# Kernel tuning notes

Hardware: AMD Instinct MI355X
Metric: run time of the kernel (lower is better)

Reference implementation:

```python
import jax, jax.numpy as jnp
import numpy as np
from jax import lax

D, H, DH, F, K, L, N = 512, 8, 64, 2048, 31, 512, 16
EPS = 1e-5

def layer_norm(x, g, b):
    m = x.mean(-1, keepdims=True)
    v = ((x - m) ** 2).mean(-1, keepdims=True)
    return (x - m) / jnp.sqrt(v + EPS) * g + b

def swish(x):
    return x * jax.nn.sigmoid(x)

def ffn(x, w1, b1, w2, b2):
    return swish(x @ w1.T + b1) @ w2.T + b2

def rel_shift(x):
    # x: (N,H,T,2T-1) -> (N,H,T,T); out[...,i,j] = x[...,i, T-1-i+j]
    T = x.shape[2]
    rows = jnp.arange(T)[:, None]
    cols = (T - 1) - rows + jnp.arange(T)[None, :]
    return x[:, :, rows, cols]

def rel_attn(x, pos_emb, in_w, in_b, out_w, out_b, pos_w, bu, bv):
    Lq, Nb, E = x.shape
    qkv = x @ in_w.T + in_b  # (L,N,3E)
    q, k, v = jnp.split(qkv, 3, axis=-1)
    q = q.reshape(Lq, Nb, H, DH).transpose(1, 2, 0, 3)  # (N,H,L,DH)
    k = k.reshape(Lq, Nb, H, DH).transpose(1, 2, 0, 3)
    v = v.reshape(Lq, Nb, H, DH).transpose(1, 2, 0, 3)
    p = (pos_emb[0] @ pos_w.T).reshape(-1, H, DH).transpose(1, 0, 2)  # (H,2L-1,DH)
    scaling = DH ** -0.5
    q_u = q + bu[None, :, None, :]
    q_v = q + bv[None, :, None, :]
    matrix_ac = jnp.einsum('nhld,nhsd->nhls', q_u, k)        # (N,H,L,L)
    matrix_bd = jnp.einsum('nhld,hmd->nhlm', q_v, p)         # (N,H,L,2L-1)
    matrix_bd = rel_shift(matrix_bd)                         # (N,H,L,L)
    attn = jax.nn.softmax((matrix_ac + matrix_bd) * scaling, axis=-1)
    out = jnp.einsum('nhls,nhsd->nhld', attn, v)
    out = out.transpose(2, 0, 1, 3).reshape(Lq, Nb, E)
    return out @ out_w.T + out_b

def conv_module(x, pw1_w, pw1_b, dw_w, dw_b, g, b, mean, var, pw2_w, pw2_b):
    # x: (L,N,C) -> (N,C,L)
    y = x.transpose(1, 2, 0)
    y = jnp.einsum('ncl,oc->nol', y, pw1_w) + pw1_b[None, :, None]
    a, gate = jnp.split(y, 2, axis=1)
    y = a * jax.nn.sigmoid(gate)  # GLU over channel dim
    pad = (K - 1) // 2
    y = lax.conv_general_dilated(y, dw_w[:, None, :], (1,), [(pad, pad)],
                                 feature_group_count=D,
                                 dimension_numbers=('NCH', 'OIH', 'NCH'))
    y = y + dw_b[None, :, None]
    # BatchNorm1d in eval mode with running stats
    y = (y - mean[None, :, None]) / jnp.sqrt(var[None, :, None] + EPS)
    y = y * g[None, :, None] + b[None, :, None]
    y = swish(y)
    y = jnp.einsum('ncl,oc->nol', y, pw2_w) + pw2_b[None, :, None]
    return y.transpose(2, 0, 1)  # back to (L,N,C)

def setup_inputs() -> dict:
    key = jax.random.key(0)
    ks = iter(jax.random.split(key, 64))
    def nrm(shape, s=0.02):
        return jax.random.normal(next(ks), shape, dtype=jnp.float32) * s
    return {
        'src': jax.random.normal(next(ks), (L, N, D), dtype=jnp.float32),
        'pos_emb': jax.random.normal(next(ks), (1, 2 * L - 1, D), dtype=jnp.float32),
        'ffm_w1': nrm((F, D)), 'ffm_b1': jnp.zeros((F,), jnp.float32),
        'ffm_w2': nrm((D, F)), 'ffm_b2': jnp.zeros((D,), jnp.float32),
        'ff_w1': nrm((F, D)), 'ff_b1': jnp.zeros((F,), jnp.float32),
        'ff_w2': nrm((D, F)), 'ff_b2': jnp.zeros((D,), jnp.float32),
        'in_proj_w': nrm((3 * D, D)), 'in_proj_b': jnp.zeros((3 * D,), jnp.float32),
        'out_proj_w': nrm((D, D)), 'out_proj_b': jnp.zeros((D,), jnp.float32),
        'pos_w': nrm((D, D)),
        'pos_bias_u': nrm((H, DH)), 'pos_bias_v': nrm((H, DH)),
        'conv_pw1_w': nrm((2 * D, D)), 'conv_pw1_b': jnp.zeros((2 * D,), jnp.float32),
        'conv_dw_w': nrm((D, K)), 'conv_dw_b': jnp.zeros((D,), jnp.float32),
        'bn_gamma': jnp.ones((D,), jnp.float32), 'bn_beta': jnp.zeros((D,), jnp.float32),
        'bn_mean': jnp.zeros((D,), jnp.float32), 'bn_var': jnp.ones((D,), jnp.float32),
        'conv_pw2_w': nrm((D, D)), 'conv_pw2_b': jnp.zeros((D,), jnp.float32),
        'ln_ffm_g': jnp.ones((D,), jnp.float32), 'ln_ffm_b': jnp.zeros((D,), jnp.float32),
        'ln_mha_g': jnp.ones((D,), jnp.float32), 'ln_mha_b': jnp.zeros((D,), jnp.float32),
        'ln_conv_g': jnp.ones((D,), jnp.float32), 'ln_conv_b': jnp.zeros((D,), jnp.float32),
        'ln_ff_g': jnp.ones((D,), jnp.float32), 'ln_ff_b': jnp.zeros((D,), jnp.float32),
        'ln_final_g': jnp.ones((D,), jnp.float32), 'ln_final_b': jnp.zeros((D,), jnp.float32),
    }

def reference(src, pos_emb, ffm_w1, ffm_b1, ffm_w2, ffm_b2, ff_w1, ff_b1, ff_w2, ff_b2,
              in_proj_w, in_proj_b, out_proj_w, out_proj_b, pos_w, pos_bias_u, pos_bias_v,
              conv_pw1_w, conv_pw1_b, conv_dw_w, conv_dw_b, bn_gamma, bn_beta, bn_mean, bn_var,
              conv_pw2_w, conv_pw2_b, ln_ffm_g, ln_ffm_b, ln_mha_g, ln_mha_b, ln_conv_g, ln_conv_b,
              ln_ff_g, ln_ff_b, ln_final_g, ln_final_b):
    # pre-norm conformer block, ff_scale = 0.5, dropout omitted (eval)
    x = src
    x = x + 0.5 * ffn(layer_norm(x, ln_ffm_g, ln_ffm_b), ffm_w1, ffm_b1, ffm_w2, ffm_b2)
    x = x + rel_attn(layer_norm(x, ln_mha_g, ln_mha_b), pos_emb,
                     in_proj_w, in_proj_b, out_proj_w, out_proj_b,
                     pos_w, pos_bias_u, pos_bias_v)
    x = x + conv_module(layer_norm(x, ln_conv_g, ln_conv_b),
                        conv_pw1_w, conv_pw1_b, conv_dw_w, conv_dw_b,
                        bn_gamma, bn_beta, bn_mean, bn_var, conv_pw2_w, conv_pw2_b)
    x = x + 0.5 * ffn(layer_norm(x, ln_ff_g, ln_ff_b), ff_w1, ff_b1, ff_w2, ff_b2)
    return layer_norm(x, ln_final_g, ln_final_b)
```

## Files before the change

kernel.cpp:

```cpp
#include <hip/hip_runtime.h>
#include <cstdint>
#include <cstddef>

typedef unsigned short u16;
typedef __attribute__((ext_vector_type(4))) float f32x4;
typedef __attribute__((ext_vector_type(8))) short bf16x8;
typedef __attribute__((ext_vector_type(8))) unsigned short u16x8;

__device__ __forceinline__ float sigm(float x) { return 1.f / (1.f + __expf(-x)); }
__device__ __forceinline__ float bf2f(u16 u) {
    union { unsigned int i; float f; } c; c.i = ((unsigned int)u) << 16; return c.f;
}
__device__ __forceinline__ u16 f2bf(float f) {
    union { float f; unsigned int i; } c; c.f = f;
    unsigned int x = c.i;
    x += 0x7fffu + ((x >> 16) & 1u);
    return (u16)(x >> 16);
}


__global__ void castall_k(const float* __restrict__ s0, const float* __restrict__ s1,
                          const float* __restrict__ s2, const float* __restrict__ s3,
                          const float* __restrict__ s4, const float* __restrict__ s5,
                          const float* __restrict__ s6, const float* __restrict__ s7,
                          const float* __restrict__ s8, const float* __restrict__ s9,
                          u16* __restrict__ dst) {
    int i = blockIdx.x * 256 + threadIdx.x;
    if (i >= 6815232) return;
    const float* s; int off;
    if      (i < 1048576) { s = s0; off = 0; }
    else if (i < 2097152) { s = s1; off = 1048576; }
    else if (i < 3145728) { s = s2; off = 2097152; }
    else if (i < 4194304) { s = s3; off = 3145728; }
    else if (i < 4980736) { s = s4; off = 4194304; }
    else if (i < 5242880) { s = s5; off = 4980736; }
    else if (i < 5767168) { s = s6; off = 5242880; }
    else if (i < 6029312) { s = s7; off = 5767168; }
    else if (i < 6291456) { s = s8; off = 6029312; }
    else                  { s = s9; off = 6291456; }
    dst[i] = f2bf(s[i - off]);
}

template <bool OUTBF>
__global__ __launch_bounds__(256) void ln512_k(const float* __restrict__ x,
                                               const float* __restrict__ g,
                                               const float* __restrict__ b,
                                               void* __restrict__ outv) {
    int row = blockIdx.x * 4 + (threadIdx.x >> 6);
    int lane = threadIdx.x & 63;
    const float* xr = x + (size_t)row * 512 + lane * 8;
    float4 v0 = *(const float4*)(xr);
    float4 v1 = *(const float4*)(xr + 4);
    float va[8] = {v0.x, v0.y, v0.z, v0.w, v1.x, v1.y, v1.z, v1.w};
    float s = 0.f;
#pragma unroll
    for (int t = 0; t < 8; t++) s += va[t];
#pragma unroll
    for (int o = 32; o > 0; o >>= 1) s += __shfl_xor(s, o);
    float m = s * (1.0f / 512.0f);
    float q = 0.f;
#pragma unroll
    for (int t = 0; t < 8; t++) { float d = va[t] - m; q += d * d; }
#pragma unroll
    for (int o = 32; o > 0; o >>= 1) q += __shfl_xor(q, o);
    float inv = rsqrtf(q * (1.0f / 512.0f) + 1e-5f);
    int cb = lane * 8;
    if (OUTBF) {
        u16* o = (u16*)outv + (size_t)row * 512 + cb;
#pragma unroll
        for (int t = 0; t < 8; t++)
            o[t] = f2bf((va[t] - m) * inv * g[cb + t] + b[cb + t]);
    } else {
        float* o = (float*)outv + (size_t)row * 512 + cb;
#pragma unroll
        for (int t = 0; t < 8; t++)
            o[t] = (va[t] - m) * inv * g[cb + t] + b[cb + t];
    }
}

__global__ __launch_bounds__(256) void mgemm64_k(
    const u16* __restrict__ A, const u16* __restrict__ B, const float* __restrict__ bias,
    const float* __restrict__ add, void* __restrict__ Cv,
    int M, int Nn, int Kk, float coef, int act, int outbf) {
    __shared__ u16 lA[2][2048];
    __shared__ u16 lB[2][2048];
    int tid = threadIdx.x;
    int lane = tid & 63;
    int w = tid >> 6;
    int quad = lane >> 4, rl = lane & 15;
    int wm = (w >> 1) * 32, wn = (w & 1) * 32;
    int m0 = blockIdx.x << 6, n0 = blockIdx.y << 6;

    f32x4 acc[2][2];
#pragma unroll
    for (int i = 0; i < 2; i++)
#pragma unroll
        for (int j = 0; j < 2; j++) acc[i][j] = (f32x4){0.f, 0.f, 0.f, 0.f};

    int srow = tid >> 2;
    int scol = (tid & 3) << 3;
    const u16* gA = A + (size_t)(m0 + srow) * Kk + scol;
    const u16* gB = B + (size_t)(n0 + srow) * Kk + scol;
    int lso = tid * 8;
    int lra = wm * 32 + rl * 32 + quad * 8;
    int lrb = wn * 32 + rl * 32 + quad * 8;

    auto STAGE = [&](int buf, int k0) {
        __builtin_amdgcn_global_load_lds(
            (const __attribute__((address_space(1))) void*)(gA + k0),
            (__attribute__((address_space(3))) void*)(lA[buf] + lso), 16, 0, 0);
        __builtin_amdgcn_global_load_lds(
            (const __attribute__((address_space(1))) void*)(gB + k0),
            (__attribute__((address_space(3))) void*)(lB[buf] + lso), 16, 0, 0);
    };
    auto COMP = [&](int buf) {
        bf16x8 af[2], bf[2];
#pragma unroll
        for (int t = 0; t < 2; t++) {
            af[t] = *(const bf16x8*)(lA[buf] + lra + t * 512);
            bf[t] = *(const bf16x8*)(lB[buf] + lrb + t * 512);
        }
#pragma unroll
        for (int i = 0; i < 2; i++)
#pragma unroll
            for (int j = 0; j < 2; j++)
                acc[i][j] = __builtin_amdgcn_mfma_f32_16x16x32_bf16(af[i], bf[j], acc[i][j], 0, 0, 0);
    };

    int nk = Kk >> 5;
    STAGE(0, 0);
    __syncthreads();
    for (int kt = 1; kt < nk; kt++) {
        STAGE(kt & 1, kt << 5);
        COMP((kt - 1) & 1);
        __syncthreads();
    }
    COMP((nk - 1) & 1);

    int rbase = quad * 4;
#pragma unroll
    for (int i = 0; i < 2; i++) {
#pragma unroll
        for (int j = 0; j < 2; j++) {
            int n = n0 + wn + j * 16 + rl;
            float bv = bias ? bias[n] : 0.f;
#pragma unroll
            for (int r = 0; r < 4; r++) {
                int m = m0 + wm + i * 16 + rbase + r;
                float c = acc[i][j][r] + bv;
                if (act == 1) c *= sigm(c);
                size_t o = (size_t)m * Nn + n;
                if (add) c = add[o] + coef * c;
                if (outbf) ((u16*)Cv)[o] = f2bf(c);
                else ((float*)Cv)[o] = c;
            }
        }
    }
}

__global__ __launch_bounds__(256) void mgemmglu_k(
    const u16* __restrict__ A, const u16* __restrict__ B, const float* __restrict__ bias,
    u16* __restrict__ Cv, int Kk) {
    __shared__ u16 lA[2][2048];
    __shared__ u16 lBa[2][2048];
    __shared__ u16 lBg[2][2048];
    int tid = threadIdx.x;
    int lane = tid & 63;
    int w = tid >> 6;
    int quad = lane >> 4, rl = lane & 15;
    int wm = (w >> 1) * 32, wn = (w & 1) * 32;
    int m0 = blockIdx.x << 6, n0 = blockIdx.y << 6;

    f32x4 accA[2][2], accG[2][2];
#pragma unroll
    for (int i = 0; i < 2; i++)
#pragma unroll
        for (int j = 0; j < 2; j++) {
            accA[i][j] = (f32x4){0.f, 0.f, 0.f, 0.f};
            accG[i][j] = (f32x4){0.f, 0.f, 0.f, 0.f};
        }

    int srow = tid >> 2;
    int scol = (tid & 3) << 3;
    const u16* gA  = A + (size_t)(m0 + srow) * Kk + scol;
    const u16* gBa = B + (size_t)(n0 + srow) * Kk + scol;
    const u16* gBg = B + (size_t)(512 + n0 + srow) * Kk + scol;
    int lso = tid * 8;
    int lra = wm * 32 + rl * 32 + quad * 8;
    int lrb = wn * 32 + rl * 32 + quad * 8;

    auto STAGE = [&](int buf, int k0) {
        __builtin_amdgcn_global_load_lds(
            (const __attribute__((address_space(1))) void*)(gA + k0),
            (__attribute__((address_space(3))) void*)(lA[buf] + lso), 16, 0, 0);
        __builtin_amdgcn_global_load_lds(
            (const __attribute__((address_space(1))) void*)(gBa + k0),
            (__attribute__((address_space(3))) void*)(lBa[buf] + lso), 16, 0, 0);
        __builtin_amdgcn_global_load_lds(
            (const __attribute__((address_space(1))) void*)(gBg + k0),
            (__attribute__((address_space(3))) void*)(lBg[buf] + lso), 16, 0, 0);
    };
    auto COMP = [&](int buf) {
        bf16x8 af[2], ba[2], bg[2];
#pragma unroll
        for (int t = 0; t < 2; t++) {
            af[t] = *(const bf16x8*)(lA[buf] + lra + t * 512);
            ba[t] = *(const bf16x8*)(lBa[buf] + lrb + t * 512);
            bg[t] = *(const bf16x8*)(lBg[buf] + lrb + t * 512);
        }
#pragma unroll
        for (int i = 0; i < 2; i++)
#pragma unroll
            for (int j = 0; j < 2; j++) {
                accA[i][j] = __builtin_amdgcn_mfma_f32_16x16x32_bf16(af[i], ba[j], accA[i][j], 0, 0, 0);
                accG[i][j] = __builtin_amdgcn_mfma_f32_16x16x32_bf16(af[i], bg[j], accG[i][j], 0, 0, 0);
            }
    };

    int nk = Kk >> 5;
    STAGE(0, 0);
    __syncthreads();
    for (int kt = 1; kt < nk; kt++) {
        STAGE(kt & 1, kt << 5);
        COMP((kt - 1) & 1);
        __syncthreads();
    }
    COMP((nk - 1) & 1);

    int rbase = quad * 4;
#pragma unroll
    for (int i = 0; i < 2; i++) {
#pragma unroll
        for (int j = 0; j < 2; j++) {
            int n = n0 + wn + j * 16 + rl;
            float bva = bias[n], bvg = bias[512 + n];
#pragma unroll
            for (int r = 0; r < 4; r++) {
                int m = m0 + wm + i * 16 + rbase + r;
                float a = accA[i][j][r] + bva;
                float g = accG[i][j][r] + bvg;
                Cv[(size_t)m * 512 + n] = f2bf(a * sigm(g));
            }
        }
    }
}

__global__ __launch_bounds__(256) void posb_k(const u16* __restrict__ A,
                                              const u16* __restrict__ B,
                                              u16* __restrict__ Pbf) {
    __shared__ u16 lA[4096];
    __shared__ u16 lB[4096];
    const int Kk = 512;
    int tid = threadIdx.x;
    int lane = tid & 63, w = tid >> 6;
    int wm = (w >> 1) * 64, wn = (w & 1) * 64;
    int m0 = blockIdx.x << 7, n0 = blockIdx.y << 7;

    f32x4 acc[4][4];
#pragma unroll
    for (int i = 0; i < 4; i++)
#pragma unroll
        for (int j = 0; j < 4; j++) acc[i][j] = (f32x4){0.f, 0.f, 0.f, 0.f};

    int srow = tid >> 2;
    int scol = (tid & 3) << 3;
    int ar0 = m0 + srow;       if (ar0 > 1022) ar0 = 1022;
    int ar1 = m0 + 64 + srow;  if (ar1 > 1022) ar1 = 1022;
    const u16* gA0 = A + (size_t)ar0 * Kk + scol;
    const u16* gA1 = A + (size_t)ar1 * Kk + scol;
    const u16* gB = B + (size_t)(n0 + srow) * Kk + scol;
    int lso = tid * 8;
    int lra = wm * 32 + (lane & 15) * 32 + (lane >> 4) * 8;
    int lrb = wn * 32 + (lane & 15) * 32 + (lane >> 4) * 8;

    for (int k0 = 0; k0 < Kk; k0 += 32) {
        __builtin_amdgcn_global_load_lds(
            (const __attribute__((address_space(1))) void*)(gA0 + k0),
            (__attribute__((address_space(3))) void*)(lA + lso), 16, 0, 0);
        __builtin_amdgcn_global_load_lds(
            (const __attribute__((address_space(1))) void*)(gA1 + k0),
            (__attribute__((address_space(3))) void*)(lA + 2048 + lso), 16, 0, 0);
        __builtin_amdgcn_global_load_lds(
            (const __attribute__((address_space(1))) void*)(gB + k0),
            (__attribute__((address_space(3))) void*)(lB + lso), 16, 0, 0);
        __builtin_amdgcn_global_load_lds(
            (const __attribute__((address_space(1))) void*)(gB + (size_t)64 * Kk + k0),
            (__attribute__((address_space(3))) void*)(lB + 2048 + lso), 16, 0, 0);
        __syncthreads();
        bf16x8 af[4], bf[4];
#pragma unroll
        for (int t = 0; t < 4; t++) {
            af[t] = *(const bf16x8*)(lA + lra + t * 512);
            bf[t] = *(const bf16x8*)(lB + lrb + t * 512);
        }
#pragma unroll
        for (int i = 0; i < 4; i++)
#pragma unroll
            for (int j = 0; j < 4; j++)
                acc[i][j] = __builtin_amdgcn_mfma_f32_16x16x32_bf16(af[i], bf[j], acc[i][j], 0, 0, 0);
        __syncthreads();
    }

    int rbase = (lane >> 4) * 4;
    int ncol = lane & 15;
#pragma unroll
    for (int i = 0; i < 4; i++) {
#pragma unroll
        for (int j = 0; j < 4; j++) {
            int n = n0 + wn + j * 16 + ncol;
            int h = n >> 6, d = n & 63;
#pragma unroll
            for (int r = 0; r < 4; r++) {
                int m = m0 + wm + i * 16 + rbase + r;
                u16 val = (m < 1023) ? f2bf(acc[i][j][r]) : (u16)0;
                Pbf[(((size_t)(h * 1024 + m)) << 6) + d] = val;
            }
        }
    }
}

__global__ __launch_bounds__(256) void fattn_k(
    const u16* __restrict__ QU, const u16* __restrict__ QV,
    const u16* __restrict__ Kb, const u16* __restrict__ Pbf,
    const u16* __restrict__ VT, u16* __restrict__ ctx) {
    __shared__ u16 arr[19072];
    u16* sRect = arr;
    u16* sP = arr;
    u16* sCtx = arr + 16768;
    float* sRed = (float*)(arr + 18816);

    int tid = threadIdx.x;
    int lane = tid & 63, w = tid >> 6;
    int quad = lane >> 4, col = lane & 15;
    int nh = blockIdx.x, h = nh & 7, nb = nh >> 3;
    int m0 = blockIdx.y << 5;
    int nlo = 480 - m0;

    const u16* QVz = QV + ((size_t)nh << 15);
    const u16* QUz = QU + ((size_t)nh << 15);
    const u16* Kz  = Kb + ((size_t)nh << 15);
    const u16* Vz  = VT + ((size_t)nh << 15);
    const u16* Pb  = Pbf + ((size_t)h << 16);

    bf16x8 av[2][2];
#pragma unroll
    for (int ks = 0; ks < 2; ks++)
#pragma unroll
        for (int t = 0; t < 2; t++)
            av[ks][t] = *(const bf16x8*)(QVz + ((size_t)(m0 + t * 16 + col) << 6) + (ks << 5) + quad * 8);
#pragma unroll
    for (int idx = 0; idx < 9; idx++) {
        int nt = w + (idx << 2);
        if (nt < 34) {
            int crow = nt * 16 + col;
            const u16* pb = Pb + ((size_t)(nlo + crow) << 6) + quad * 8;
            f32x4 b0 = (f32x4){0.f, 0.f, 0.f, 0.f};
            f32x4 b1 = (f32x4){0.f, 0.f, 0.f, 0.f};
#pragma unroll
            for (int ks = 0; ks < 2; ks++) {
                bf16x8 bfr = *(const bf16x8*)(pb + (ks << 5));
                b0 = __builtin_amdgcn_mfma_f32_16x16x32_bf16(av[ks][0], bfr, b0, 0, 0, 0);
                b1 = __builtin_amdgcn_mfma_f32_16x16x32_bf16(av[ks][1], bfr, b1, 0, 0, 0);
            }
#pragma unroll
            for (int r = 0; r < 4; r++) {
                int ml0 = quad * 4 + r;
                int j0 = crow + ml0 - 31;
                if (j0 >= 0 && j0 < 512) sRect[ml0 * 524 + j0] = f2bf(b0[r]);
                int ml1 = ml0 + 16;
                int j1 = crow + ml1 - 31;
                if (j1 >= 0 && j1 < 512) sRect[ml1 * 524 + j1] = f2bf(b1[r]);
            }
        }
    }

    bf16x8 au[2][2];
#pragma unroll
    for (int ks = 0; ks < 2; ks++)
#pragma unroll
        for (int t = 0; t < 2; t++)
            au[ks][t] = *(const bf16x8*)(QUz + ((size_t)(m0 + t * 16 + col) << 6) + (ks << 5) + quad * 8);
    f32x4 ac[2][8];
#pragma unroll
    for (int t = 0; t < 2; t++)
#pragma unroll
        for (int jt = 0; jt < 8; jt++) ac[t][jt] = (f32x4){0.f, 0.f, 0.f, 0.f};
#pragma unroll
    for (int jt = 0; jt < 8; jt++) {
        const u16* kp = Kz + ((size_t)((w << 7) + jt * 16 + col) << 6) + quad * 8;
#pragma unroll
        for (int ks = 0; ks < 2; ks++) {
            bf16x8 bfr = *(const bf16x8*)(kp + (ks << 5));
            ac[0][jt] = __builtin_amdgcn_mfma_f32_16x16x32_bf16(au[ks][0], bfr, ac[0][jt], 0, 0, 0);
            ac[1][jt] = __builtin_amdgcn_mfma_f32_16x16x32_bf16(au[ks][1], bfr, ac[1][jt], 0, 0, 0);
        }
    }
    __syncthreads();

    float rmax[2][4];
#pragma unroll
    for (int t = 0; t < 2; t++)
#pragma unroll
        for (int r = 0; r < 4; r++) rmax[t][r] = -1e30f;
#pragma unroll
    for (int jt = 0; jt < 8; jt++) {
        int j = (w << 7) + jt * 16 + col;
#pragma unroll
        for (int t = 0; t < 2; t++)
#pragma unroll
            for (int r = 0; r < 4; r++) {
                int ml = t * 16 + quad * 4 + r;
                float v = (ac[t][jt][r] + bf2f(sRect[ml * 524 + j])) * 0.125f;
                ac[t][jt][r] = v;
                rmax[t][r] = fmaxf(rmax[t][r], v);
            }
    }
#pragma unroll
    for (int o = 1; o <= 8; o <<= 1)
#pragma unroll
        for (int t = 0; t < 2; t++)
#pragma unroll
            for (int r = 0; r < 4; r++) rmax[t][r] = fmaxf(rmax[t][r], __shfl_xor(rmax[t][r], o));
    if (col == 0)
#pragma unroll
        for (int t = 0; t < 2; t++)
#pragma unroll
            for (int r = 0; r < 4; r++) sRed[(t * 16 + quad * 4 + r) * 4 + w] = rmax[t][r];
    __syncthreads();
    float gmax[2][4], psum[2][4];
#pragma unroll
    for (int t = 0; t < 2; t++)
#pragma unroll
        for (int r = 0; r < 4; r++) {
            int ml = t * 16 + quad * 4 + r;
            gmax[t][r] = fmaxf(fmaxf(sRed[ml * 4 + 0], sRed[ml * 4 + 1]),
                               fmaxf(sRed[ml * 4 + 2], sRed[ml * 4 + 3]));
            psum[t][r] = 0.f;
        }
    __syncthreads();
#pragma unroll
    for (int jt = 0; jt < 8; jt++)
#pragma unroll
        for (int t = 0; t < 2; t++)
#pragma unroll
            for (int r = 0; r < 4; r++) {
                float e = __expf(ac[t][jt][r] - gmax[t][r]);
                ac[t][jt][r] = e;
                psum[t][r] += e;
            }
#pragma unroll
    for (int o = 1; o <= 8; o <<= 1)
#pragma unroll
        for (int t = 0; t < 2; t++)
#pragma unroll
            for (int r = 0; r < 4; r++) psum[t][r] += __shfl_xor(psum[t][r], o);
    if (col == 0)
#pragma unroll
        for (int t = 0; t < 2; t++)
#pragma unroll
            for (int r = 0; r < 4; r++) sRed[(t * 16 + quad * 4 + r) * 4 + w] = psum[t][r];
    __syncthreads();
    float rinv[2][4];
#pragma unroll
    for (int t = 0; t < 2; t++)
#pragma unroll
        for (int r = 0; r < 4; r++) {
            int ml = t * 16 + quad * 4 + r;
            rinv[t][r] = 1.f / (sRed[ml * 4 + 0] + sRed[ml * 4 + 1] + sRed[ml * 4 + 2] + sRed[ml * 4 + 3]);
        }

#pragma unroll
    for (int jt = 0; jt < 8; jt++) {
        int j = (w << 7) + jt * 16 + col;
#pragma unroll
        for (int t = 0; t < 2; t++)
#pragma unroll
            for (int r = 0; r < 4; r++)
                sP[(t * 16 + quad * 4 + r) * 520 + j] = f2bf(ac[t][jt][r] * rinv[t][r]);
    }
    __syncthreads();

    f32x4 cacc[2];
    cacc[0] = (f32x4){0.f, 0.f, 0.f, 0.f};
    cacc[1] = (f32x4){0.f, 0.f, 0.f, 0.f};
    {
        const u16* vp = Vz + ((size_t)((w << 4) + col) << 9) + quad * 8;
#pragma unroll
        for (int kc = 0; kc < 2; kc++)
#pragma unroll
            for (int s2 = 0; s2 < 8; s2++) {
                int ko = (kc << 8) + (s2 << 5);
                bf16x8 a0 = *(const bf16x8*)(sP + col * 520 + ko + quad * 8);
                bf16x8 a1 = *(const bf16x8*)(sP + (col + 16) * 520 + ko + quad * 8);
                bf16x8 bfr = *(const bf16x8*)(vp + ko);
                cacc[0] = __builtin_amdgcn_mfma_f32_16x16x32_bf16(a0, bfr, cacc[0], 0, 0, 0);
                cacc[1] = __builtin_amdgcn_mfma_f32_16x16x32_bf16(a1, bfr, cacc[1], 0, 0, 0);
            }
    }

#pragma unroll
    for (int t = 0; t < 2; t++)
#pragma unroll
        for (int r = 0; r < 4; r++)
            sCtx[(t * 16 + quad * 4 + r) * 64 + (w << 4) + col] = f2bf(cacc[t][r]);
    __syncthreads();
    {
        int row = tid >> 3, seg = tid & 7;
        u16* dst = ctx + (((size_t)((m0 + row) * 16 + nb)) << 9) + (h << 6) + seg * 8;
        *(uint4*)dst = *(const uint4*)(sCtx + row * 64 + seg * 8);
    }
}

__global__ __launch_bounds__(256) void repack_k(const u16* __restrict__ qkv,
                                                const float* __restrict__ bu,
                                                const float* __restrict__ bv,
                                                u16* __restrict__ QU, u16* __restrict__ QV,
                                                u16* __restrict__ Kb, u16* __restrict__ VT) {
    __shared__ u16 sV[64 * 72];
    int nh = blockIdx.x, h = nh & 7, n = nh >> 3;
    int l0 = blockIdx.y << 6;
    int tid = threadIdx.x;
    int d8 = (tid & 7) << 3;
    float bub[8], bvb[8];
#pragma unroll
    for (int e = 0; e < 8; e++) {
        bub[e] = bu[h * 64 + d8 + e];
        bvb[e] = bv[h * 64 + d8 + e];
    }
#pragma unroll
    for (int rep = 0; rep < 2; rep++) {
        int ll = (tid >> 3) + rep * 32;
        int l = l0 + ll;
        size_t base = (size_t)(l * 16 + n) * 1536 + h * 64 + d8;
        u16x8 q = *(const u16x8*)(qkv + base);
        u16x8 k = *(const u16x8*)(qkv + base + 512);
        u16x8 v = *(const u16x8*)(qkv + base + 1024);
        u16x8 qu, qv;
#pragma unroll
        for (int e = 0; e < 8; e++) {
            float qf = bf2f(q[e]);
            qu[e] = f2bf(qf + bub[e]);
            qv[e] = f2bf(qf + bvb[e]);
        }
        size_t o = ((size_t)nh * 512 + l) * 64 + d8;
        *(u16x8*)(QU + o) = qu;
        *(u16x8*)(QV + o) = qv;
        *(u16x8*)(Kb + o) = k;
        *(u16x8*)(sV + ll * 72 + d8) = v;
    }
    __syncthreads();
    int d = tid >> 2, ls = (tid & 3) << 4;
    u16 tmp[16];
#pragma unroll
    for (int e = 0; e < 16; e++) tmp[e] = sV[(ls + e) * 72 + d];
    u16* dst = VT + ((size_t)nh * 64 + d) * 512 + l0 + ls;
    *(u16x8*)(dst) = *(const u16x8*)(tmp);
    *(u16x8*)(dst + 8) = *(const u16x8*)(tmp + 8);
}

__global__ __launch_bounds__(256) void dwconv_k(
    const u16* __restrict__ g, const float* __restrict__ w, const float* __restrict__ wb,
    const float* __restrict__ bng, const float* __restrict__ bnb, const float* __restrict__ bnm,
    const float* __restrict__ bnv, u16* __restrict__ out) {
    int idx = blockIdx.x * 256 + threadIdx.x;
    int c = idx & 511;
    int t = idx >> 9;
    int n = t & 15, l0 = (t >> 4) << 4;
    float win[46];
#pragma unroll
    for (int q = 0; q < 46; q++) {
        int ll = l0 - 15 + q;
        win[q] = (ll >= 0 && ll < 512) ? bf2f(g[((size_t)(ll * 16 + n) << 9) + c]) : 0.f;
    }
    float wgt[31];
#pragma unroll
    for (int k = 0; k < 31; k++) wgt[k] = w[c * 31 + k];
    float ivg = rsqrtf(bnv[c] + 1e-5f) * bng[c];
    float mc = bnm[c], bc = bnb[c], wbc = wb[c];
#pragma unroll
    for (int r = 0; r < 16; r++) {
        float acc = 0.f;
#pragma unroll
        for (int k = 0; k < 31; k++) acc += wgt[k] * win[r + k];
        acc += wbc;
        float y = (acc - mc) * ivg + bc;
        y = y * sigm(y);
        out[((size_t)((l0 + r) * 16 + n) << 9) + c] = f2bf(y);
    }
}

extern "C" void kernel_launch(void* const* d_in, const int* in_sizes, int n_in,
                              void* d_out, int out_size, void* d_ws, size_t ws_size,
                              hipStream_t stream) {
    const float* src      = (const float*)d_in[0];
    const float* pos_emb  = (const float*)d_in[1];
    const float* ffm_w1   = (const float*)d_in[2];
    const float* ffm_b1   = (const float*)d_in[3];
    const float* ffm_w2   = (const float*)d_in[4];
    const float* ffm_b2   = (const float*)d_in[5];
    const float* ff_w1    = (const float*)d_in[6];
    const float* ff_b1    = (const float*)d_in[7];
    const float* ff_w2    = (const float*)d_in[8];
    const float* ff_b2    = (const float*)d_in[9];
    const float* in_w     = (const float*)d_in[10];
    const float* in_b     = (const float*)d_in[11];
    const float* out_w    = (const float*)d_in[12];
    const float* out_b    = (const float*)d_in[13];
    const float* pos_w    = (const float*)d_in[14];
    const float* bu       = (const float*)d_in[15];
    const float* bv       = (const float*)d_in[16];
    const float* pw1_w    = (const float*)d_in[17];
    const float* pw1_b    = (const float*)d_in[18];
    const float* dw_w     = (const float*)d_in[19];
    const float* dw_b     = (const float*)d_in[20];
    const float* bng      = (const float*)d_in[21];
    const float* bnb      = (const float*)d_in[22];
    const float* bnm      = (const float*)d_in[23];
    const float* bnv      = (const float*)d_in[24];
    const float* pw2_w    = (const float*)d_in[25];
    const float* pw2_b    = (const float*)d_in[26];
    const float* ln_ffm_g = (const float*)d_in[27];
    const float* ln_ffm_b = (const float*)d_in[28];
    const float* ln_mha_g = (const float*)d_in[29];
    const float* ln_mha_b = (const float*)d_in[30];
    const float* ln_cv_g  = (const float*)d_in[31];
    const float* ln_cv_b  = (const float*)d_in[32];
    const float* ln_ff_g  = (const float*)d_in[33];
    const float* ln_ff_b  = (const float*)d_in[34];
    const float* ln_fin_g = (const float*)d_in[35];
    const float* ln_fin_b = (const float*)d_in[36];
    (void)in_sizes; (void)n_in; (void)out_size; (void)ws_size;

    const size_t MEG = 1048576;
    u16* U = (u16*)d_ws;
    float* xA = (float*)U;
    u16* Pbf = U;
    float* xB = (float*)(U + 8 * MEG);
    u16* LNB = U + 16 * MEG;
    u16* BIG = U + 20 * MEG;
    u16* QU = U + 36 * MEG;
    u16* QV = U + 40 * MEG;
    u16* Kb = U + 44 * MEG;
    u16* VT = U + 48 * MEG;
    u16* WB = U + 52 * MEG;
    u16* w_ffm1 = WB;
    u16* w_ffm2 = WB + 1 * MEG;
    u16* w_ff1  = WB + 2 * MEG;
    u16* w_ff2  = WB + 3 * MEG;
    u16* w_in   = WB + 4 * MEG;
    u16* w_out  = WB + 4 * MEG + 786432;
    u16* w_pw1  = WB + 5 * MEG;
    u16* w_pw2  = WB + 5 * MEG + 524288;
    u16* w_pos  = WB + 6029312;
    u16* w_pe   = WB + 6291456;
    u16* CTX = LNB;
    u16* GLU = QU;
    u16* CACT = QV;

    castall_k<<<26622, 256, 0, stream>>>(ffm_w1, ffm_w2, ff_w1, ff_w2, in_w, out_w,
                                         pw1_w, pw2_w, pos_w, pos_emb, WB);

    ln512_k<true><<<2048, 256, 0, stream>>>(src, ln_ffm_g, ln_ffm_b, LNB);
    mgemm64_k<<<dim3(128, 32), 256, 0, stream>>>(LNB, w_ffm1, ffm_b1, nullptr, BIG,
                                                 8192, 2048, 512, 0.f, 1, 1);
    mgemm64_k<<<dim3(128, 8), 256, 0, stream>>>(BIG, w_ffm2, ffm_b2, src, xB,
                                                8192, 512, 2048, 0.5f, 0, 0);

    ln512_k<true><<<2048, 256, 0, stream>>>(xB, ln_mha_g, ln_mha_b, LNB);
    posb_k<<<dim3(8, 4), 256, 0, stream>>>(w_pe, w_pos, Pbf);
    mgemm64_k<<<dim3(128, 24), 256, 0, stream>>>(LNB, w_in, in_b, nullptr, BIG,
                                                 8192, 1536, 512, 0.f, 0, 1);
    repack_k<<<dim3(128, 8), 256, 0, stream>>>(BIG, bu, bv, QU, QV, Kb, VT);
    fattn_k<<<dim3(128, 16), 256, 0, stream>>>(QU, QV, Kb, Pbf, VT, CTX);
    mgemm64_k<<<dim3(128, 8), 256, 0, stream>>>(CTX, w_out, out_b, xB, xA,
                                                8192, 512, 512, 1.f, 0, 0);

    ln512_k<true><<<2048, 256, 0, stream>>>(xA, ln_cv_g, ln_cv_b, LNB);
    mgemmglu_k<<<dim3(128, 8), 256, 0, stream>>>(LNB, w_pw1, pw1_b, GLU, 512);
    dwconv_k<<<1024, 256, 0, stream>>>(GLU, dw_w, dw_b, bng, bnb, bnm, bnv, CACT);
    mgemm64_k<<<dim3(128, 8), 256, 0, stream>>>(CACT, w_pw2, pw2_b, xA, xB,
                                                8192, 512, 512, 1.f, 0, 0);

    ln512_k<true><<<2048, 256, 0, stream>>>(xB, ln_ff_g, ln_ff_b, LNB);
    mgemm64_k<<<dim3(128, 32), 256, 0, stream>>>(LNB, w_ff1, ff_b1, nullptr, BIG,
                                                 8192, 2048, 512, 0.f, 1, 1);
    mgemm64_k<<<dim3(128, 8), 256, 0, stream>>>(BIG, w_ff2, ff_b2, xB, xA,
                                                8192, 512, 2048, 0.5f, 0, 0);

    ln512_k<false><<<2048, 256, 0, stream>>>(xA, ln_fin_g, ln_fin_b, (float*)d_out);
}
```

Measured before the change: 524.2 us.

## Split GEMM K across two waves with per-wave 64x64 tiles and LDS reduction

Replaces the 4-wave 64x64-tile GEMM with a 2-wave kernel. Each wave computes the full 64x64 output tile over half of K using 4x4 MFMA fragments and its own private LDS double buffer, synchronised with per-wave vmcnt waits instead of block barriers. The two partial sums are reduced through LDS before the fused epilogue. This is meant to raise MFMA work per LDS fragment load and remove block-level barriers from the main loop, at the cost of more accumulator registers, fewer waves per block, and an extra LDS reduction pass.

```diff
diff --git a/kernel.cpp b/kernel.cpp
--- a/kernel.cpp
+++ b/kernel.cpp
@@ -78,82 +78,95 @@
     }
 }
 
-__global__ __launch_bounds__(256) void mgemm64_k(
+__global__ __launch_bounds__(128) void mgemmsk_k(
     const u16* __restrict__ A, const u16* __restrict__ B, const float* __restrict__ bias,
     const float* __restrict__ add, void* __restrict__ Cv,
     int M, int Nn, int Kk, float coef, int act, int outbf) {
-    __shared__ u16 lA[2][2048];
-    __shared__ u16 lB[2][2048];
+    __shared__ u16 sh[16384];
     int tid = threadIdx.x;
-    int lane = tid & 63;
-    int w = tid >> 6;
+    int lane = tid & 63, w = tid >> 6;
     int quad = lane >> 4, rl = lane & 15;
-    int wm = (w >> 1) * 32, wn = (w & 1) * 32;
     int m0 = blockIdx.x << 6, n0 = blockIdx.y << 6;
-
-    f32x4 acc[2][2];
-#pragma unroll
-    for (int i = 0; i < 2; i++)
-#pragma unroll
-        for (int j = 0; j < 2; j++) acc[i][j] = (f32x4){0.f, 0.f, 0.f, 0.f};
-
-    int srow = tid >> 2;
-    int scol = (tid & 3) << 3;
-    const u16* gA = A + (size_t)(m0 + srow) * Kk + scol;
-    const u16* gB = B + (size_t)(n0 + srow) * Kk + scol;
-    int lso = tid * 8;
-    int lra = wm * 32 + rl * 32 + quad * 8;
-    int lrb = wn * 32 + rl * 32 + quad * 8;
+    int Kh = Kk >> 1;
+    int kb = w * Kh;
+
+    f32x4 acc[4][4];
+#pragma unroll
+    for (int i = 0; i < 4; i++)
+#pragma unroll
+        for (int j = 0; j < 4; j++) acc[i][j] = (f32x4){0.f, 0.f, 0.f, 0.f};
+
+    int srow = lane >> 2;
+    int scol = (lane & 3) << 3;
+    const u16* gAs = A + (size_t)(m0 + srow) * Kk + kb + scol;
+    const u16* gBs = B + (size_t)(n0 + srow) * Kk + kb + scol;
+    u16* myA = sh + (w << 13);
+    u16* myB = myA + 4096;
+    int lso = lane << 3;
 
     auto STAGE = [&](int buf, int k0) {
-        __builtin_amdgcn_global_load_lds(
-            (const __attribute__((address_space(1))) void*)(gA + k0),
-            (__attribute__((address_space(3))) void*)(lA[buf] + lso), 16, 0, 0);
-        __builtin_amdgcn_global_load_lds(
-            (const __attribute__((address_space(1))) void*)(gB + k0),
-            (__attribute__((address_space(3))) void*)(lB[buf] + lso), 16, 0, 0);
+#pragma unroll
+        for (int i = 0; i < 4; i++) {
+            __builtin_amdgcn_global_load_lds(
+                (const __attribute__((address_space(1))) void*)(gAs + (size_t)(i * 16) * Kk + k0),
+                (__attribute__((address_space(3))) void*)(myA + (buf << 11) + (i << 9) + lso), 16, 0, 0);
+            __builtin_amdgcn_global_load_lds(
+                (const __attribute__((address_space(1))) void*)(gBs + (size_t)(i * 16) * Kk + k0),
+                (__attribute__((address_space(3))) void*)(myB + (buf << 11) + (i << 9) + lso), 16, 0, 0);
+        }
     };
     auto COMP = [&](int buf) {
-        bf16x8 af[2], bf[2];
-#pragma unroll
-        for (int t = 0; t < 2; t++) {
-            af[t] = *(const bf16x8*)(lA[buf] + lra + t * 512);
-            bf[t] = *(const bf16x8*)(lB[buf] + lrb + t * 512);
-        }
-#pragma unroll
-        for (int i = 0; i < 2; i++)
-#pragma unroll
-            for (int j = 0; j < 2; j++)
+        bf16x8 af[4], bf[4];
+#pragma unroll
+        for (int t = 0; t < 4; t++) {
+            af[t] = *(const bf16x8*)(myA + (buf << 11) + (t * 16 + rl) * 32 + quad * 8);
+            bf[t] = *(const bf16x8*)(myB + (buf << 11) + (t * 16 + rl) * 32 + quad * 8);
+        }
+#pragma unroll
+        for (int i = 0; i < 4; i++)
+#pragma unroll
+            for (int j = 0; j < 4; j++)
                 acc[i][j] = __builtin_amdgcn_mfma_f32_16x16x32_bf16(af[i], bf[j], acc[i][j], 0, 0, 0);
     };
 
-    int nk = Kk >> 5;
+    int nk = Kh >> 5;
     STAGE(0, 0);
-    __syncthreads();
+    asm volatile("s_waitcnt vmcnt(0)" ::: "memory");
     for (int kt = 1; kt < nk; kt++) {
         STAGE(kt & 1, kt << 5);
         COMP((kt - 1) & 1);
-        __syncthreads();
+        asm volatile("s_waitcnt vmcnt(0)" ::: "memory");
     }
     COMP((nk - 1) & 1);
 
-    int rbase = quad * 4;
-#pragma unroll
-    for (int i = 0; i < 2; i++) {
-#pragma unroll
-        for (int j = 0; j < 2; j++) {
-            int n = n0 + wn + j * 16 + rl;
-            float bv = bias ? bias[n] : 0.f;
-#pragma unroll
-            for (int r = 0; r < 4; r++) {
-                int m = m0 + wm + i * 16 + rbase + r;
-                float c = acc[i][j][r] + bv;
-                if (act == 1) c *= sigm(c);
-                size_t o = (size_t)m * Nn + n;
-                if (add) c = add[o] + coef * c;
-                if (outbf) ((u16*)Cv)[o] = f2bf(c);
-                else ((float*)Cv)[o] = c;
-            }
+    float* part = (float*)(sh) + (w << 12);
+#pragma unroll
+    for (int i = 0; i < 4; i++)
+#pragma unroll
+        for (int j = 0; j < 4; j++)
+#pragma unroll
+            for (int r = 0; r < 4; r++)
+                part[(i * 16 + quad * 4 + r) * 64 + j * 16 + rl] = acc[i][j][r];
+    __syncthreads();
+    const float* p0 = (const float*)sh;
+    const float* p1 = (const float*)sh + 4096;
+    int cc = (lane & 15) << 2;
+    int r0 = (w << 5) + (lane >> 4);
+#pragma unroll
+    for (int s = 0; s < 8; s++) {
+        int lrow = r0 + (s << 2);
+        f32x4 v0 = *(const f32x4*)(p0 + lrow * 64 + cc);
+        f32x4 v1 = *(const f32x4*)(p1 + lrow * 64 + cc);
+        int m = m0 + lrow;
+        int n = n0 + cc;
+#pragma unroll
+        for (int r = 0; r < 4; r++) {
+            float c = v0[r] + v1[r] + (bias ? bias[n + r] : 0.f);
+            if (act == 1) c *= sigm(c);
+            size_t o = (size_t)m * Nn + n + r;
+            if (add) c = add[o] + coef * c;
+            if (outbf) ((u16*)Cv)[o] = f2bf(c);
+            else ((float*)Cv)[o] = c;
         }
     }
 }
@@ -661,30 +674,30 @@
                                          pw1_w, pw2_w, pos_w, pos_emb, WB);
 
     ln512_k<true><<<2048, 256, 0, stream>>>(src, ln_ffm_g, ln_ffm_b, LNB);
-    mgemm64_k<<<dim3(128, 32), 256, 0, stream>>>(LNB, w_ffm1, ffm_b1, nullptr, BIG,
+    mgemmsk_k<<<dim3(128, 32), 128, 0, stream>>>(LNB, w_ffm1, ffm_b1, nullptr, BIG,
                                                  8192, 2048, 512, 0.f, 1, 1);
-    mgemm64_k<<<dim3(128, 8), 256, 0, stream>>>(BIG, w_ffm2, ffm_b2, src, xB,
+    mgemmsk_k<<<dim3(128, 8), 128, 0, stream>>>(BIG, w_ffm2, ffm_b2, src, xB,
                                                 8192, 512, 2048, 0.5f, 0, 0);
 
     ln512_k<true><<<2048, 256, 0, stream>>>(xB, ln_mha_g, ln_mha_b, LNB);
     posb_k<<<dim3(8, 4), 256, 0, stream>>>(w_pe, w_pos, Pbf);
-    mgemm64_k<<<dim3(128, 24), 256, 0, stream>>>(LNB, w_in, in_b, nullptr, BIG,
+    mgemmsk_k<<<dim3(128, 24), 128, 0, stream>>>(LNB, w_in, in_b, nullptr, BIG,
                                                  8192, 1536, 512, 0.f, 0, 1);
     repack_k<<<dim3(128, 8), 256, 0, stream>>>(BIG, bu, bv, QU, QV, Kb, VT);
     fattn_k<<<dim3(128, 16), 256, 0, stream>>>(QU, QV, Kb, Pbf, VT, CTX);
-    mgemm64_k<<<dim3(128, 8), 256, 0, stream>>>(CTX, w_out, out_b, xB, xA,
+    mgemmsk_k<<<dim3(128, 8), 128, 0, stream>>>(CTX, w_out, out_b, xB, xA,
                                                 8192, 512, 512, 1.f, 0, 0);
 
     ln512_k<true><<<2048, 256, 0, stream>>>(xA, ln_cv_g, ln_cv_b, LNB);
     mgemmglu_k<<<dim3(128, 8), 256, 0, stream>>>(LNB, w_pw1, pw1_b, GLU, 512);
     dwconv_k<<<1024, 256, 0, stream>>>(GLU, dw_w, dw_b, bng, bnb, bnm, bnv, CACT);
-    mgemm64_k<<<dim3(128, 8), 256, 0, stream>>>(CACT, w_pw2, pw2_b, xA, xB,
+    mgemmsk_k<<<dim3(128, 8), 128, 0, stream>>>(CACT, w_pw2, pw2_b, xA, xB,
                                                 8192, 512, 512, 1.f, 0, 0);
 
     ln512_k<true><<<2048, 256, 0, stream>>>(xB, ln_ff_g, ln_ff_b, LNB);
-    mgemm64_k<<<dim3(128, 32), 256, 0, stream>>>(LNB, w_ff1, ff_b1, nullptr, BIG,
+    mgemmsk_k<<<dim3(128, 32), 128, 0, stream>>>(LNB, w_ff1, ff_b1, nullptr, BIG,
                                                  8192, 2048, 512, 0.f, 1, 1);
-    mgemm64_k<<<dim3(128, 8), 256, 0, stream>>>(BIG, w_ff2, ff_b2, xB, xA,
+    mgemmsk_k<<<dim3(128, 8), 128, 0, stream>>>(BIG, w_ff2, ff_b2, xB, xA,
                                                 8192, 512, 2048, 0.5f, 0, 0);
 
     ln512_k<false><<<2048, 256, 0, stream>>>(xA, ln_fin_g, ln_fin_b, (float*)d_out);
```

Result: slower. 637.9 us (+21.7%).
